# Kernel optimization log

Measured on AMD Instinct MI355X. Metric: run time of the kernel, lower is better.

Reference implementation:

```python
import jax, jax.numpy as jnp
import numpy as np

# DCNv3 hyperparameters (from init_kwargs)
K = 3           # kernel_size
STRIDE = 1
PAD = 1
DIL = 1
GROUP = 4
GC = 16         # internelchannels = group_channels
CH = GROUP * GC # 64 internal channels
P = K * K       # sampling points per group
OFFSET_SCALE = 1.0


def setup_inputs() -> dict:
    key = jax.random.key(0)
    ks = jax.random.split(key, 8)
    B, H, W = 4, 128, 128
    cop_ch, aop_ch, out_ch = 64, 64, 64
    return {
        "x1": jax.random.normal(ks[0], (B, cop_ch, H, W), jnp.float32),
        "x2": jax.random.normal(ks[1], (B, aop_ch, H, W), jnp.float32),
        # value input projection (COP stream)
        "w_value": jax.random.normal(ks[2], (cop_ch, CH), jnp.float32) / np.sqrt(cop_ch),
        "b_value": jnp.zeros((CH,), jnp.float32),
        # offset/mask feature conv (AOP stream)
        "w_conv": jax.random.normal(ks[3], (K, K, aop_ch, CH), jnp.float32) / np.sqrt(K * K * aop_ch),
        "b_conv": jnp.zeros((CH,), jnp.float32),
        # offset head (small init so sampling stays near the regular grid)
        "w_offset": jax.random.normal(ks[4], (CH, GROUP * P * 2), jnp.float32) * 0.01,
        "b_offset": jnp.zeros((GROUP * P * 2,), jnp.float32),
        # mask head (softmax-normalized modulation)
        "w_mask": jax.random.normal(ks[5], (CH, GROUP * P), jnp.float32) * 0.1,
        "b_mask": jnp.zeros((GROUP * P,), jnp.float32),
        # output projection
        "w_out": jax.random.normal(ks[6], (CH, out_ch), jnp.float32) / np.sqrt(CH),
        "b_out": jnp.zeros((out_ch,), jnp.float32),
    }


def _bilinear_sample(vflat, x, y, Hp, Wp):
    """vflat: [B, Hp*Wp, G, gc]; x, y: [B, N, G] pixel coords in padded image.
    Returns [B, N, G, gc] zero-padded bilinear samples (grid_sample align_corners=False)."""
    x0 = jnp.floor(x)
    y0 = jnp.floor(y)
    out = jnp.zeros(vflat.shape[:1] + x.shape[1:] + vflat.shape[-1:], vflat.dtype)
    for dy in (0, 1):
        for dx in (0, 1):
            xi = x0 + dx
            yi = y0 + dy
            wgt = (1.0 - jnp.abs(x - xi)) * (1.0 - jnp.abs(y - yi))
            valid = (xi >= 0) & (xi < Wp) & (yi >= 0) & (yi < Hp)
            idx = (jnp.clip(yi, 0, Hp - 1) * Wp + jnp.clip(xi, 0, Wp - 1)).astype(jnp.int32)
            v = jnp.take_along_axis(vflat, idx[..., None], axis=1)  # [B,N,G,gc]
            out = out + v * (wgt * valid.astype(wgt.dtype))[..., None]
    return out


def reference(x1, x2, w_value, b_value, w_conv, b_conv,
              w_offset, b_offset, w_mask, b_mask, w_out, b_out):
    # NCHW -> NHWC (as in the torch wrapper)
    cop = jnp.transpose(x1, (0, 2, 3, 1))
    aop = jnp.transpose(x2, (0, 2, 3, 1))
    B, H, W, _ = cop.shape
    Hout = (H + 2 * PAD - DIL * (K - 1) - 1) // STRIDE + 1
    Wout = (W + 2 * PAD - DIL * (K - 1) - 1) // STRIDE + 1

    # value projection from COP stream: [B,H,W,CH]
    value = cop @ w_value + b_value

    # offset/mask branch from AOP stream
    feat = jax.lax.conv_general_dilated(
        aop, w_conv, (STRIDE, STRIDE), [(PAD, PAD), (PAD, PAD)],
        dimension_numbers=("NHWC", "HWIO", "NHWC")) + b_conv
    feat = jax.nn.gelu(feat)                                  # [B,Hout,Wout,CH]
    offset = (feat @ w_offset + b_offset).reshape(B, Hout, Wout, GROUP, P, 2)
    mask = jax.nn.softmax(
        (feat @ w_mask + b_mask).reshape(B, Hout, Wout, GROUP, P), axis=-1)

    # zero-pad the value map (DCNv3 pads input then samples in padded coords)
    vp = jnp.pad(value, ((0, 0), (PAD, PAD), (PAD, PAD), (0, 0)))
    Hp, Wp = H + 2 * PAD, W + 2 * PAD
    vflat = vp.reshape(B, Hp * Wp, GROUP, GC)

    # reference points + dilation grid (pixel coords in padded image)
    ref_x = (DIL * (K - 1) / 2 + jnp.arange(Wout, dtype=jnp.float32) * STRIDE)
    ref_y = (DIL * (K - 1) / 2 + jnp.arange(Hout, dtype=jnp.float32) * STRIDE)
    ky, kx = jnp.meshgrid(jnp.arange(K) - (K - 1) // 2,
                          jnp.arange(K) - (K - 1) // 2, indexing="ij")
    grid = jnp.stack([kx, ky], -1).reshape(P, 2).astype(jnp.float32) * DIL  # (dx,dy)

    x = (ref_x[None, None, :, None, None] + grid[None, None, None, None, :, 0]
         + offset[..., 0] * OFFSET_SCALE)                     # [B,Hout,Wout,G,P]
    y = (ref_y[None, :, None, None, None] + grid[None, None, None, None, :, 1]
         + offset[..., 1] * OFFSET_SCALE)

    # flatten to [B, N, G] with N = Hout*Wout*P (group axis kept last for gather)
    xr = jnp.transpose(x, (0, 1, 2, 4, 3)).reshape(B, Hout * Wout * P, GROUP)
    yr = jnp.transpose(y, (0, 1, 2, 4, 3)).reshape(B, Hout * Wout * P, GROUP)

    sampled = _bilinear_sample(vflat, xr, yr, Hp, Wp)         # [B,N,G,gc]
    sampled = sampled.reshape(B, Hout, Wout, P, GROUP, GC)

    out = jnp.einsum("bhwpgc,bhwgp->bhwgc", sampled, mask).reshape(B, Hout, Wout, CH)
    out = out @ w_out + b_out                                 # [B,Hout,Wout,out_ch]
    return jnp.transpose(out, (0, 3, 1, 2))                   # NHWC -> NCHW
```

## Files before the change

kernel.cpp:

```cpp
#include <hip/hip_runtime.h>
#include <cstdint>
#include <cstddef>

typedef float f4 __attribute__((ext_vector_type(4)));
typedef float f2 __attribute__((ext_vector_type(2)));
typedef float f32x4 __attribute__((ext_vector_type(4)));
typedef short short8 __attribute__((ext_vector_type(8)));
typedef unsigned int u32;
typedef unsigned short u16;
typedef u32 u32x4 __attribute__((ext_vector_type(4)));


__device__ __forceinline__ u16 f2bf(float f) {
    u32 u = __builtin_bit_cast(u32, f);
    return (u16)((u + 0x7FFFu + ((u >> 16) & 1u)) >> 16);
}

__device__ __forceinline__ int xcd_swz10(int d) {
    return ((d & 7) << 7) | (d >> 3);
}
__device__ __forceinline__ int xcd_swz11(int d) {
    return ((d & 7) << 8) | (d >> 3);
}

__global__ __launch_bounds__(256) void prep_zero_k(float* __restrict__ vpad,
                                                   char* __restrict__ x2tp) {
    int blk = blockIdx.x;
    if (blk < 260) {
        int i = blk * 256 + threadIdx.x;
        if (i >= 66560) return;
        int c4 = i & 15;
        int rest = i >> 4;
        int b = rest / 1040;
        int e = rest - b * 1040;
        int y, x;
        if (e < 132)      { y = 0;   x = e; }
        else if (e < 264) { y = 1;   x = e - 132; }
        else if (e < 396) { y = 130; x = e - 264; }
        else if (e < 528) { y = 131; x = e - 396; }
        else { int e2 = e - 528; y = 2 + (e2 >> 2); int m = e2 & 3;
               x = (m < 2) ? m : m + 128; }
        f4 z = {0.f, 0.f, 0.f, 0.f};
        *(f4*)(vpad + (((size_t)b * 17424 + (size_t)y * 132 + x) * 64 + c4 * 4)) = z;
    } else {
        int i = (blk - 260) * 256 + threadIdx.x;
        if (i >= 16512) return;
        int c8 = i & 7;
        int rest = i >> 3;
        int b = rest / 516;
        int e = rest - b * 516;
        int y, x;
        if (e < 130)      { y = 0;       x = e; }
        else if (e < 260) { y = 129;     x = e - 130; }
        else if (e < 388) { y = e - 259; x = 0; }
        else              { y = e - 387; x = 129; }
        u32x4 z = {0u, 0u, 0u, 0u};
        *(u32x4*)(x2tp + ((size_t)b * 16900 + (size_t)y * 130 + x) * 128 + c8 * 16) = z;
    }
}

__global__ __launch_bounds__(256) void prep_w_k(const float* __restrict__ wc,
                                                const float* __restrict__ wo,
                                                const float* __restrict__ wm,
                                                char* __restrict__ wbfT,
                                                char* __restrict__ whead) {
    int blk = blockIdx.x;
    if (blk < 72) {
        int i = blk * 256 + threadIdx.x;
        int c = i / 288, kp = i - c * 288;
        int k = kp << 1;
        float f0 = wc[(size_t)k * 64 + c];
        float f1 = wc[(size_t)(k + 1) * 64 + c];
        u32 pk = (u32)f2bf(f0) | ((u32)f2bf(f1) << 16);
        *(u32*)(wbfT + (size_t)c * 1152 + kp * 4) = pk;
    } else {
        int i = (blk - 72) * 256 + threadIdx.x;
        int k = i & 63, col = i >> 6;
        float v = 0.f;
        if (col < 72)       v = wo[(size_t)k * 72 + col];
        else if (col < 108) v = wm[(size_t)k * 36 + col - 72];
        *(u16*)(whead + (size_t)(col * 64 + k) * 2) = f2bf(v);
    }
}

__global__ __launch_bounds__(256) void x2prep_k(const float* __restrict__ x2,
                                                char* __restrict__ x2tp) {
    __shared__ u32 tr[4096];
    int t = threadIdx.x;
    int y = blockIdx.x & 127, b = blockIdx.x >> 7;
    const float* xb = x2 + (size_t)b * 64 * 16384 + (size_t)y * 128;
    #pragma unroll 4
    for (int j = 0; j < 16; j++) {
        int idx = t + (j << 8);
        int x = idx & 127, cip = idx >> 7;
        int ci = cip << 1;
        float f0 = xb[(size_t)ci * 16384 + x];
        float f1 = xb[(size_t)(ci + 1) * 16384 + x];
        u32 pk = (u32)f2bf(f0) | ((u32)f2bf(f1) << 16);
        int key = (x + 1) & 7;
        int byt = x * 128 + (((ci >> 3) ^ key) << 4) + (ci & 7) * 2;
        tr[byt >> 2] = pk;
    }
    __syncthreads();
    const u32x4* src = (const u32x4*)tr;
    u32x4* dst = (u32x4*)(x2tp + ((size_t)(b * 130 + y + 1) * 130 + 1) * 128);
    #pragma unroll
    for (int j = 0; j < 4; j++) {
        int c = t + (j << 8);
        dst[c] = src[c];
    }
}

__global__ __launch_bounds__(256) void value_proj_k(const float* __restrict__ x1,
                                                    const float* __restrict__ wv,
                                                    const float* __restrict__ bv,
                                                    float* __restrict__ vpad) {
    __shared__ float xs[64][64];
    __shared__ float wsh[64][64];
    int tid = threadIdx.x;
    int bidx = xcd_swz10(blockIdx.x);
    int xb = bidx & 1;
    int y  = (bidx >> 1) & 127;
    int b  = bidx >> 8;
    int x0 = xb * 64;

    for (int j = 0; j < 16; j++) {
        int idx = tid + j * 256;
        int ci = idx >> 6, px = idx & 63;
        xs[ci][px]  = x1[(((size_t)b * 64 + ci) * 128 + y) * 128 + x0 + px];
        wsh[ci][px] = wv[idx];
    }
    __syncthreads();

    int c0 = (tid & 15) * 4, p0 = (tid >> 4) * 4;
    f4 bb = *(const f4*)(bv + c0);
    f4 acc[4];
    #pragma unroll
    for (int i = 0; i < 4; i++) acc[i] = bb;

    #pragma unroll
    for (int ci = 0; ci < 64; ci++) {
        f4 w4 = *(f4*)&wsh[ci][c0];
        f4 x4 = *(f4*)&xs[ci][p0];
        #pragma unroll
        for (int i = 0; i < 4; i++) acc[i] += x4[i] * w4;
    }

    #pragma unroll
    for (int i = 0; i < 4; i++) {
        int xp = x0 + p0 + i + 2;
        *(f4*)(vpad + (((size_t)b * 132 + (y + 2)) * 132 + xp) * 64 + c0) = acc[i];
    }
}

__global__ __launch_bounds__(256, 4) void conv_mfma_k(const char* __restrict__ x2tp,
                                                      const char* __restrict__ wbfT,
                                                      const float* __restrict__ bc,
                                                      char* __restrict__ featb) {
    __shared__ char slab[3 * 8448];
    int tid = threadIdx.x;
    int l = tid & 63, w = tid >> 6;
    int bidx = xcd_swz10(blockIdx.x);
    int xb = bidx & 1, y = (bidx >> 1) & 127, b = bidx >> 8;
    int x0 = xb << 6;

    const char* gr = x2tp + ((size_t)(b * 130 + y) * 130 + x0) * 128;
    for (int q = w; q < 27; q += 4) {
        int r = q / 9, cq = q - r * 9;
        int nb = (cq < 8) ? 1024 : 256;
        if (l * 16 < nb) {
            const char* g = gr + (size_t)r * (130 * 128) + cq * 1024 + l * 16;
            char* p = slab + r * 8448 + cq * 1024 + l * 16;
            __builtin_amdgcn_global_load_lds(
                (const __attribute__((address_space(1))) u32*)g,
                (__attribute__((address_space(3))) u32*)p, 16, 0, 0);
        }
    }
    __syncthreads();

    int m0 = w << 4;
    int r16 = l & 15, g16 = l >> 4;
    f32x4 acc[4] = {{0.f,0.f,0.f,0.f},{0.f,0.f,0.f,0.f},
                    {0.f,0.f,0.f,0.f},{0.f,0.f,0.f,0.f}};
    const char* wb = wbfT + (size_t)r16 * 1152 + g16 * 16;

    #pragma unroll
    for (int s = 0; s < 18; s++) {
        const int t9 = s >> 1;
        const int ky = t9 / 3, kx = t9 - ky * 3;
        const int ci0g = (s & 1) * 4;
        int x_sl = m0 + r16 + kx;
        int go = (ci0g + g16) ^ (x_sl & 7);
        short8 a = *(const short8*)(slab + ky * 8448 + x_sl * 128 + go * 16);
        #pragma unroll
        for (int cb = 0; cb < 4; cb++) {
            short8 bf = *(const short8*)(wb + (size_t)cb * (16 * 1152) + s * 64);
            acc[cb] = __builtin_amdgcn_mfma_f32_16x16x32_bf16(a, bf, acc[cb], 0, 0, 0);
        }
    }

    const float kA = 0.7978845608028654f, kB = 0.044715f;
    char* fp = featb + ((size_t)b * 16384 + (size_t)y * 128 + x0 + m0) * 128;
    #pragma unroll
    for (int cb = 0; cb < 4; cb++) {
        float bcv = bc[cb * 16 + r16];
        #pragma unroll
        for (int j = 0; j < 4; j++) {
            float v = acc[cb][j] + bcv;
            float z = kA * (v + kB * v * v * v);
            float e = __expf(2.f * z);
            float th = 1.f - 2.f / (e + 1.f);
            float o = 0.5f * v * (1.f + th);
            *(u16*)(fp + (size_t)(g16 * 4 + j) * 128 + (cb * 16 + r16) * 2) = f2bf(o);
        }
    }
}

__global__ __launch_bounds__(256, 6) void dcn_fused_v5(const char* __restrict__ featb,
                                                       const float* __restrict__ vpad,
                                                       const char* __restrict__ whead,
                                                       const float* __restrict__ bo,
                                                       const float* __restrict__ bm,
                                                       const float* __restrict__ wout,
                                                       const float* __restrict__ bout,
                                                       float* __restrict__ out) {
    __shared__ float off_s [4][8][74];
    __shared__ float msk_s [4][8][38];
    __shared__ float samp_s[4][8][64];

    int tid = threadIdx.x;
    int w = tid >> 6, l = tid & 63;
    int blk = xcd_swz11(blockIdx.x);
    int b = blk >> 9, y = (blk >> 2) & 127, xq = blk & 3;
    int x0w = xq * 32 + w * 8;
    int pix0 = ((b << 7) + y) * 128 + x0w;

    int r = l & 15, q = l >> 4;

    const char* fpt = featb + (size_t)(pix0 + r) * 128 + q * 16;
    short8 a0 = *(const short8*)fpt;
    short8 a1 = *(const short8*)(fpt + 64);

    const char* wh = whead + (size_t)r * 128 + q * 16;
    f32x4 hc[7];
    #pragma unroll
    for (int t = 0; t < 7; t++) {
        short8 b0 = *(const short8*)(wh + t * 2048);
        short8 b1 = *(const short8*)(wh + t * 2048 + 64);
        f32x4 z = {0.f, 0.f, 0.f, 0.f};
        z = __builtin_amdgcn_mfma_f32_16x16x32_bf16(a0, b0, z, 0, 0, 0);
        hc[t] = __builtin_amdgcn_mfma_f32_16x16x32_bf16(a1, b1, z, 0, 0, 0);
    }

    if (q < 2) {
        #pragma unroll
        for (int t = 0; t < 7; t++) {
            int col = t * 16 + r;
            float bias = 0.f;
            if (col < 72)        bias = bo[col];
            else if (col < 108)  bias = bm[col - 72];
            #pragma unroll
            for (int j = 0; j < 4; j++) {
                int px = q * 4 + j;
                float v = hc[t][j] + bias;
                if (col < 72)       off_s[w][px][col] = v;
                else if (col < 108) msk_s[w][px][col - 72] = v;
            }
        }
    }

    if (l < 32) {
        int px = l >> 2, g = l & 3;
        float m[9];
        #pragma unroll
        for (int p = 0; p < 9; p++) m[p] = msk_s[w][px][g * 9 + p];
        float mx = m[0];
        #pragma unroll
        for (int p = 1; p < 9; p++) mx = fmaxf(mx, m[p]);
        float s = 0.f;
        #pragma unroll
        for (int p = 0; p < 9; p++) { m[p] = __expf(m[p] - mx); s += m[p]; }
        float inv = 1.f / s;
        #pragma unroll
        for (int p = 0; p < 9; p++) msk_s[w][px][g * 9 + p] = m[p] * inv;
    }

    {
        int cc4 = l & 3, g = (l >> 2) & 3, pxs = l >> 4;
        const float* vb = vpad + (size_t)b * 17424 * 64 + g * 16 + cc4 * 4;
        #pragma unroll
        for (int j = 0; j < 2; j++) {
            int px = pxs * 2 + j;
            int xpix = x0w + px;
            f4 acc = {0.f, 0.f, 0.f, 0.f};
            #pragma unroll
            for (int p = 0; p < 9; p++) {
                const int kx = p % 3, ky = p / 3;
                f2 oxy = *(const f2*)&off_s[w][px][g * 18 + 2 * p];
                float mv = msk_s[w][px][g * 9 + p];
                float sx = (float)(xpix + kx) + oxy[0];
                float sy = (float)(y + ky) + oxy[1];
                float xf = floorf(sx), yf = floorf(sy);
                float fx = sx - xf, fy = sy - yf;
                int ix = (int)xf, iy = (int)yf;
                int e0 = (iy * 132 + ix + 133) << 6;
                const float* pa = vb + e0;
                f4 v00 = *(const f4*)pa;
                f4 v01 = *(const f4*)(pa + 64);
                f4 v10 = *(const f4*)(pa + 8448);
                f4 v11 = *(const f4*)(pa + 8512);
                float wy0 = mv * (1.f - fy), wy1 = mv * fy;
                float w00 = wy0 * (1.f - fx), w01 = wy0 * fx;
                float w10 = wy1 * (1.f - fx), w11 = wy1 * fx;
                #pragma unroll
                for (int c = 0; c < 4; c++)
                    acc[c] = fmaf(w00, v00[c],
                             fmaf(w01, v01[c],
                             fmaf(w10, v10[c],
                             fmaf(w11, v11[c], acc[c]))));
            }
            *(f4*)&samp_s[w][px][g * 16 + cc4 * 4] = acc;
        }
    }

    float oa[8];
    float bv = bout[l];
    #pragma unroll
    for (int px = 0; px < 8; px++) oa[px] = bv;
    const float* pw = wout + l;
    #pragma unroll 4
    for (int k4 = 0; k4 < 16; k4++) {
        float w0 = pw[0], w1 = pw[64], w2 = pw[128], w3 = pw[192];
        pw += 256;
        #pragma unroll
        for (int px = 0; px < 8; px++) {
            f4 sv = *(f4*)&samp_s[w][px][k4 * 4];
            oa[px] = fmaf(sv[0], w0, fmaf(sv[1], w1,
                     fmaf(sv[2], w2, fmaf(sv[3], w3, oa[px]))));
        }
    }

    float* op = out + ((size_t)b * 64 + l) * 16384 + y * 128 + x0w;
    f4 o0 = {oa[0], oa[1], oa[2], oa[3]};
    f4 o1 = {oa[4], oa[5], oa[6], oa[7]};
    *(f4*)op       = o0;
    *(f4*)(op + 4) = o1;
}

extern "C" void kernel_launch(void* const* d_in, const int* in_sizes, int n_in,
                              void* d_out, int out_size, void* d_ws, size_t ws_size,
                              hipStream_t stream) {
    const float* x1       = (const float*)d_in[0];
    const float* x2       = (const float*)d_in[1];
    const float* w_value  = (const float*)d_in[2];
    const float* b_value  = (const float*)d_in[3];
    const float* w_conv   = (const float*)d_in[4];
    const float* b_conv   = (const float*)d_in[5];
    const float* w_offset = (const float*)d_in[6];
    const float* b_offset = (const float*)d_in[7];
    const float* w_mask   = (const float*)d_in[8];
    const float* b_mask   = (const float*)d_in[9];
    const float* w_out    = (const float*)d_in[10];
    const float* b_out    = (const float*)d_in[11];

    float* vpad  = (float*)d_ws;
    char*  featb = (char*)d_ws + 17842176;
    char*  x2tp  = (char*)d_ws + 26230784;
    char*  wbfT  = (char*)d_ws + 34883584;
    char*  whead = (char*)d_ws + 34957312;
    float* outp  = (float*)d_out;

    hipLaunchKernelGGL(prep_zero_k,  dim3(325),  dim3(256), 0, stream, vpad, x2tp);
    hipLaunchKernelGGL(prep_w_k,     dim3(100),  dim3(256), 0, stream,
                       w_conv, w_offset, w_mask, wbfT, whead);
    hipLaunchKernelGGL(x2prep_k,     dim3(512),  dim3(256), 0, stream, x2, x2tp);
    hipLaunchKernelGGL(value_proj_k, dim3(1024), dim3(256), 0, stream,
                       x1, w_value, b_value, vpad);
    hipLaunchKernelGGL(conv_mfma_k,  dim3(1024), dim3(256), 0, stream,
                       x2tp, wbfT, b_conv, featb);
    hipLaunchKernelGGL(dcn_fused_v5, dim3(2048), dim3(256), 0, stream,
                       featb, vpad, whead, b_offset, b_mask, w_out, b_out, outp);
}
```

Measured before the change: 198.9 us.

## Merge prep kernels, vectorise value-proj loads, shrink DCN blocks to 128 threads

Merges the zero-padding and weight-prep kernels into one launch, which removes a kernel launch. Switches the value projection's shared-memory staging to float4 loads. Halves the fused DCN kernel's block size to two waves and doubles the grid, with a matching XCD swizzle and smaller shared arrays. The goal is better occupancy and scheduling granularity in the main kernel, at the cost of more blocks and a changed launch-bounds hint.

Result: no change. 202.2 us (+1.6%).

```diff
diff --git a/kernel.cpp b/kernel.cpp
--- a/kernel.cpp
+++ b/kernel.cpp
@@ -19,12 +19,17 @@
 __device__ __forceinline__ int xcd_swz10(int d) {
     return ((d & 7) << 7) | (d >> 3);
 }
-__device__ __forceinline__ int xcd_swz11(int d) {
-    return ((d & 7) << 8) | (d >> 3);
-}
-
-__global__ __launch_bounds__(256) void prep_zero_k(float* __restrict__ vpad,
-                                                   char* __restrict__ x2tp) {
+__device__ __forceinline__ int xcd_swz12(int d) {
+    return ((d & 7) << 9) | (d >> 3);
+}
+
+__global__ __launch_bounds__(256) void prep_all_k(float* __restrict__ vpad,
+                                                  char* __restrict__ x2tp,
+                                                  const float* __restrict__ wc,
+                                                  const float* __restrict__ wo,
+                                                  const float* __restrict__ wm,
+                                                  char* __restrict__ wbfT,
+                                                  char* __restrict__ whead) {
     int blk = blockIdx.x;
     if (blk < 260) {
         int i = blk * 256 + threadIdx.x;
@@ -42,7 +47,7 @@
                x = (m < 2) ? m : m + 128; }
         f4 z = {0.f, 0.f, 0.f, 0.f};
         *(f4*)(vpad + (((size_t)b * 17424 + (size_t)y * 132 + x) * 64 + c4 * 4)) = z;
-    } else {
+    } else if (blk < 325) {
         int i = (blk - 260) * 256 + threadIdx.x;
         if (i >= 16512) return;
         int c8 = i & 7;
@@ -56,17 +61,8 @@
         else              { y = e - 387; x = 129; }
         u32x4 z = {0u, 0u, 0u, 0u};
         *(u32x4*)(x2tp + ((size_t)b * 16900 + (size_t)y * 130 + x) * 128 + c8 * 16) = z;
-    }
-}
-
-__global__ __launch_bounds__(256) void prep_w_k(const float* __restrict__ wc,
-                                                const float* __restrict__ wo,
-                                                const float* __restrict__ wm,
-                                                char* __restrict__ wbfT,
-                                                char* __restrict__ whead) {
-    int blk = blockIdx.x;
-    if (blk < 72) {
-        int i = blk * 256 + threadIdx.x;
+    } else if (blk < 397) {
+        int i = (blk - 325) * 256 + threadIdx.x;
         int c = i / 288, kp = i - c * 288;
         int k = kp << 1;
         float f0 = wc[(size_t)k * 64 + c];
@@ -74,7 +70,7 @@
         u32 pk = (u32)f2bf(f0) | ((u32)f2bf(f1) << 16);
         *(u32*)(wbfT + (size_t)c * 1152 + kp * 4) = pk;
     } else {
-        int i = (blk - 72) * 256 + threadIdx.x;
+        int i = (blk - 397) * 256 + threadIdx.x;
         int k = i & 63, col = i >> 6;
         float v = 0.f;
         if (col < 72)       v = wo[(size_t)k * 72 + col];
@@ -124,11 +120,13 @@
     int b  = bidx >> 8;
     int x0 = xb * 64;
 
-    for (int j = 0; j < 16; j++) {
-        int idx = tid + j * 256;
-        int ci = idx >> 6, px = idx & 63;
-        xs[ci][px]  = x1[(((size_t)b * 64 + ci) * 128 + y) * 128 + x0 + px];
-        wsh[ci][px] = wv[idx];
+    #pragma unroll
+    for (int j = 0; j < 4; j++) {
+        int chunk = tid + j * 256;
+        int ci = chunk >> 4, p4 = chunk & 15;
+        *(f4*)&xs[ci][p4 * 4] =
+            *(const f4*)(x1 + (((size_t)b * 64 + ci) * 128 + y) * 128 + x0 + p4 * 4);
+        *(f4*)&wsh[ci][p4 * 4] = *(const f4*)(wv + ci * 64 + p4 * 4);
     }
     __syncthreads();
 
@@ -216,7 +214,7 @@
     }
 }
 
-__global__ __launch_bounds__(256, 6) void dcn_fused_v5(const char* __restrict__ featb,
+__global__ __launch_bounds__(128, 7) void dcn_fused_v6(const char* __restrict__ featb,
                                                        const float* __restrict__ vpad,
                                                        const char* __restrict__ whead,
                                                        const float* __restrict__ bo,
@@ -224,15 +222,15 @@
                                                        const float* __restrict__ wout,
                                                        const float* __restrict__ bout,
                                                        float* __restrict__ out) {
-    __shared__ float off_s [4][8][74];
-    __shared__ float msk_s [4][8][38];
-    __shared__ float samp_s[4][8][64];
+    __shared__ float off_s [2][8][74];
+    __shared__ float msk_s [2][8][38];
+    __shared__ float samp_s[2][8][64];
 
     int tid = threadIdx.x;
     int w = tid >> 6, l = tid & 63;
-    int blk = xcd_swz11(blockIdx.x);
-    int b = blk >> 9, y = (blk >> 2) & 127, xq = blk & 3;
-    int x0w = xq * 32 + w * 8;
+    int blk = xcd_swz12(blockIdx.x);
+    int b = blk >> 10, y = (blk >> 3) & 127, xo = blk & 7;
+    int x0w = xo * 16 + w * 8;
     int pix0 = ((b << 7) + y) * 128 + x0w;
 
     int r = l & 15, q = l >> 4;
@@ -370,14 +368,13 @@
     char*  whead = (char*)d_ws + 34957312;
     float* outp  = (float*)d_out;
 
-    hipLaunchKernelGGL(prep_zero_k,  dim3(325),  dim3(256), 0, stream, vpad, x2tp);
-    hipLaunchKernelGGL(prep_w_k,     dim3(100),  dim3(256), 0, stream,
-                       w_conv, w_offset, w_mask, wbfT, whead);
+    hipLaunchKernelGGL(prep_all_k,   dim3(425),  dim3(256), 0, stream,
+                       vpad, x2tp, w_conv, w_offset, w_mask, wbfT, whead);
     hipLaunchKernelGGL(x2prep_k,     dim3(512),  dim3(256), 0, stream, x2, x2tp);
     hipLaunchKernelGGL(value_proj_k, dim3(1024), dim3(256), 0, stream,
                        x1, w_value, b_value, vpad);
     hipLaunchKernelGGL(conv_mfma_k,  dim3(1024), dim3(256), 0, stream,
                        x2tp, wbfT, b_conv, featb);
-    hipLaunchKernelGGL(dcn_fused_v5, dim3(2048), dim3(256), 0, stream,
+    hipLaunchKernelGGL(dcn_fused_v6, dim3(4096), dim3(128), 0, stream,
                        featb, vpad, whead, b_offset, b_mask, w_out, b_out, outp);
 }
```
